# Performance work log

Hardware: AMD Instinct MI355X
Metric: run time of the kernel (lower is better)

Reference implementation:

```python
import jax, jax.numpy as jnp
import numpy as np

HEADS = 4
DH = 32            # hidden_state // multi_head = 128 // 4
HIDDEN = HEADS * DH
TEMP = float(HIDDEN) ** 0.5   # hidden_state ** alpha, alpha=0.5
BN_EPS = 1e-5


def _conv1x1(x, w, b):
    # x: [B,C,W,H], w: [O,C], b: [O] -> [B,O,W,H]
    y = jnp.einsum('oc,bcwh->bowh', w, x)
    return y + b[None, :, None, None]


def setup_inputs() -> dict:
    key = jax.random.key(0)
    ks = jax.random.split(key, 12)
    B, C, W, H = 2, 512, 64, 64
    s = lambda k, shape, scale=0.05: jax.random.normal(k, shape, jnp.float32) * scale
    return {
        'x': jax.random.normal(ks[0], (B, C, W, H), jnp.float32),
        'wq': s(ks[1], (HIDDEN, C)), 'bq': s(ks[2], (HIDDEN,)),
        'wk': s(ks[3], (HIDDEN, C)), 'bk': s(ks[4], (HIDDEN,)),
        'wv': s(ks[5], (HIDDEN, C)), 'bv': s(ks[6], (HIDDEN,)),
        'w_fuse': s(ks[7], (HEADS, HEADS), 0.5),
        'w_out': s(ks[8], (C, HIDDEN)), 'b_out': s(ks[9], (C,)),
        'bn_gamma': jnp.ones((C,), jnp.float32),
        'bn_beta': jnp.zeros((C,), jnp.float32),
        'bn_mean': s(ks[10], (C,), 0.1),
        'bn_var': jax.random.uniform(ks[11], (C,), jnp.float32, 0.5, 1.5),
    }


def reference(x, wq, bq, wk, bk, wv, bv, w_fuse, w_out, b_out,
              bn_gamma, bn_beta, bn_mean, bn_var):
    B, C, W, H = x.shape
    N = W * H
    # 1x1 conv QKV projections, split into heads
    q = _conv1x1(x, wq, bq).reshape(B, HEADS, DH, N)        # [B,h,d,N]
    q = jnp.swapaxes(q, 2, 3)                               # [B,h,N,d]
    k = _conv1x1(x, wk, bk).reshape(B, HEADS, DH, N)        # [B,h,d,N]
    v = jnp.swapaxes(_conv1x1(x, wv, bv).reshape(B, HEADS, DH, N), 2, 3)  # [B,h,N,d]
    # scaled dot-product scores
    attn = jnp.einsum('bhnd,bhdm->bhnm', q / jnp.float32(TEMP), k)  # [B,h,N,N]
    # fuse: 1x1 conv across heads on the score tensor (no bias)
    attn = jnp.einsum('gh,bhnm->bgnm', w_fuse, attn)
    attn = jax.nn.softmax(attn, axis=-1)
    # dropout is identity in eval mode
    out = jnp.einsum('bhnm,bhmd->bhnd', attn, v)            # [B,h,N,d]
    out = jnp.swapaxes(out, 2, 3).reshape(B, HIDDEN, W, H)
    out = _conv1x1(out, w_out, b_out)
    # BatchNorm2d in eval mode (running stats)
    inv = jax.lax.rsqrt(bn_var + BN_EPS)
    out = (out - bn_mean[None, :, None, None]) * (bn_gamma * inv)[None, :, None, None] \
          + bn_beta[None, :, None, None]
    return out, attn
```

## Files before the change

### kernel.cpp

```cpp
#include <hip/hip_runtime.h>
#include <hip/hip_bf16.h>
#include <cstdint>
#include <cstddef>

#define B_   2
#define C_   512
#define N_   4096
#define NH   4
#define DH_  32
#define HID  128
#define LOG2E 1.4426950408889634f

typedef __attribute__((ext_vector_type(8))) short bf16x8;
typedef __attribute__((ext_vector_type(4))) float f32x4;

#if __has_builtin(__builtin_amdgcn_exp2f)
#define EXP2(x) __builtin_amdgcn_exp2f(x)
#else
#define EXP2(x) exp2f(x)
#endif

static __device__ __forceinline__ unsigned short f2bf(float f) {
  union { float f; unsigned int u; } v; v.f = f;
  unsigned int r = v.u + 0x7fffu + ((v.u >> 16) & 1u);
  return (unsigned short)(r >> 16);
}

static __device__ __forceinline__ float sbc(float x) {
  return __uint_as_float(__builtin_amdgcn_readfirstlane(__float_as_uint(x)));
}

__global__ __launch_bounds__(256)
void prep_w(const float* __restrict__ wq, const float* __restrict__ wk,
            const float* __restrict__ wv, const float* __restrict__ wout,
            const float* __restrict__ bout, const float* __restrict__ gamma,
            const float* __restrict__ beta, const float* __restrict__ mean,
            const float* __restrict__ var,
            unsigned short* __restrict__ wbf,
            float* __restrict__ gsws, float* __restrict__ shws)
{
  if (blockIdx.x == 256) {
    int co = threadIdx.x;
#pragma unroll
    for (int i = 0; i < 2; i++, co += 256) {
      float gs = gamma[co] * rsqrtf(var[co] + 1e-5f);
      gsws[co] = gs;
      shws[co] = (bout[co] - mean[co]) * gs + beta[co];
    }
    return;
  }
  int gid  = blockIdx.x * 256 + threadIdx.x;
  int elem = gid * 4;
  int t    = elem >> 16;
  int off  = elem & 65535;
  const float* src = (t == 0) ? wq : (t == 1) ? wk : (t == 2) ? wv : wout;
  float4 v = *(const float4*)(src + off);
  alignas(8) unsigned short tmp[4];
  tmp[0] = f2bf(v.x); tmp[1] = f2bf(v.y); tmp[2] = f2bf(v.z); tmp[3] = f2bf(v.w);
  *(uint2*)(wbf + t * 65536 + off) = *(const uint2*)tmp;
}

__global__ __launch_bounds__(256)
void prep_xt(const float* __restrict__ x, unsigned short* __restrict__ xT)
{
  int bid = blockIdx.x;
  int b   = bid >> 9;
  int rem = bid & 511;
  int ct  = rem >> 6;
  int nt  = rem & 63;
  int c0  = ct << 6;
  int n0  = nt << 6;

  int tid = threadIdx.x;
  __shared__ float xs[64][65];

  const float* xb = x + (size_t)b * C_ * N_;
#pragma unroll
  for (int rr = 0; rr < 16; rr++) {
    int row = (tid >> 6) * 16 + rr;
    xs[row][tid & 63] = xb[(size_t)(c0 + row) * N_ + n0 + (tid & 63)];
  }
  __syncthreads();

  int cseg = (tid & 7) * 8;
#pragma unroll
  for (int pass = 0; pass < 2; pass++) {
    int nrow = pass * 32 + (tid >> 3);
    alignas(16) unsigned short tmp[8];
#pragma unroll
    for (int j = 0; j < 8; j++) tmp[j] = f2bf(xs[cseg + j][nrow]);
    *(uint4*)(xT + ((size_t)b * N_ + n0 + nrow) * C_ + c0 + cseg) = *(const uint4*)tmp;
  }
}

__global__ __launch_bounds__(256)
void qkv_gemm(const unsigned short* __restrict__ wbf,
              const unsigned short* __restrict__ xT,
              const float* __restrict__ bq, const float* __restrict__ bk,
              const float* __restrict__ bv,
              unsigned short* __restrict__ qws,
              unsigned short* __restrict__ kws,
              unsigned short* __restrict__ vtws)
{
  int bid = blockIdx.x;
  int ot  = bid % 6;
  int ntl = bid / 6;
  int b   = ntl >> 6;
  int n0  = (ntl & 63) << 6;
  int o0  = ot << 6;
  int t   = o0 >> 7;

  int tid = threadIdx.x;
  int w   = tid >> 6;
  int l   = tid & 63;
  int lg  = l >> 4;
  int lc  = l & 15;

  const unsigned short* xrow = xT + ((size_t)b * N_ + n0 + w * 16 + lc) * C_;
  const unsigned short* wrow0 = wbf + (size_t)(o0 + lc) * C_;

  const f32x4 zc = {0.f, 0.f, 0.f, 0.f};
  f32x4 acc[4] = {zc, zc, zc, zc};

  for (int k0 = 0; k0 < C_; k0 += 32) {
    bf16x8 bfrag = *(const bf16x8*)(xrow + k0 + lg * 8);
#pragma unroll
    for (int sub = 0; sub < 4; sub++) {
      bf16x8 afrag = *(const bf16x8*)(wrow0 + (size_t)sub * 16 * C_ + k0 + lg * 8);
      acc[sub] = __builtin_amdgcn_mfma_f32_16x16x32_bf16(afrag, bfrag, acc[sub], 0, 0, 0);
    }
  }

  const float* bias_t = (t == 0) ? bq : (t == 1) ? bk : bv;
  int n = n0 + w * 16 + lc;

#pragma unroll
  for (int sub = 0; sub < 4; sub++) {
    int oobase = (o0 & 127) + sub * 16;
    float4 bs = *(const float4*)(bias_t + oobase + lg * 4);
    float val[4];
    val[0] = acc[sub][0] + bs.x;
    val[1] = acc[sub][1] + bs.y;
    val[2] = acc[sub][2] + bs.z;
    val[3] = acc[sub][3] + bs.w;
    int h  = oobase >> 5;
    int d0 = (oobase & 31) + lg * 4;
    if (t < 2) {
      unsigned short* dst = (t == 0 ? qws : kws)
                          + (((size_t)(b * NH + h)) * N_ + n) * DH_ + d0;
      alignas(8) unsigned short tmp[4];
#pragma unroll
      for (int r = 0; r < 4; r++) tmp[r] = f2bf(val[r]);
      *(uint2*)dst = *(const uint2*)tmp;
    } else {
      unsigned short* dst = vtws + (((size_t)(b * NH + h)) * DH_ + d0) * N_ + n;
#pragma unroll
      for (int r = 0; r < 4; r++) dst[(size_t)r * N_] = f2bf(val[r]);
    }
  }
}

__global__ __launch_bounds__(512)
void attn_zpv(const unsigned short* __restrict__ qws,
              const unsigned short* __restrict__ kws,
              const unsigned short* __restrict__ vtws,
              const float* __restrict__ wfuse,
              const unsigned short* __restrict__ woutbf,
              const float* __restrict__ gsws, const float* __restrict__ shws,
              float* __restrict__ attn_out,
              float* __restrict__ out)
{
  int bid = blockIdx.x;
  int xcd = bid & 7;
  int b   = xcd >> 2;
  int qt  = (bid >> 3) * 4 + (xcd & 3);
  int n0  = qt << 4;

  int tid = threadIdx.x;
  int wv_ = tid >> 6;
  int l   = tid & 63;
  int lg  = l >> 4;
  int lc  = l & 15;

  __shared__ __align__(16) unsigned char lds_raw[8 * 4 * 16 * 40 * 2];
  unsigned short (*pbuf)[4][16][40] = (unsigned short (*)[4][16][40])lds_raw;
  float (*ored)[16][36] = (float (*)[16][36])lds_raw;
  unsigned short (*o128)[132] =
      (unsigned short (*)[132])(lds_raw + 20480);
  __shared__ float zred[8][4][4][4];

  const float TEMP = 11.313708498984761f;
  float wm[4][4];
#pragma unroll
  for (int g = 0; g < 4; g++)
#pragma unroll
    for (int h = 0; h < 4; h++)
      wm[g][h] = sbc(wfuse[g * 4 + h] * (LOG2E / TEMP));

  bf16x8 qf[4];
#pragma unroll
  for (int h = 0; h < 4; h++)
    qf[h] = *(const bf16x8*)(qws + (((size_t)(b * NH + h)) * N_ + n0 + lc) * DH_ + lg * 8);

  const f32x4 zc = {0.f, 0.f, 0.f, 0.f};

  float zp[4][4] = {};
#pragma unroll 1
  for (int pp = wv_; pp < 128; pp += 8) {
#pragma unroll
    for (int mm = 0; mm < 2; mm++) {
      int m0 = pp * 32 + mm * 16;
      f32x4 sh[4];
#pragma unroll
      for (int h = 0; h < 4; h++) {
        bf16x8 kf = *(const bf16x8*)(kws
            + (((size_t)(b * NH + h)) * N_ + m0 + lc) * DH_ + lg * 8);
        sh[h] = __builtin_amdgcn_mfma_f32_16x16x32_bf16(qf[h], kf, zc, 0, 0, 0);
      }
#pragma unroll
      for (int g = 0; g < 4; g++) {
        f32x4 sg = wm[g][0] * sh[0] + wm[g][1] * sh[1]
                 + wm[g][2] * sh[2] + wm[g][3] * sh[3];
#pragma unroll
        for (int r = 0; r < 4; r++) zp[g][r] += EXP2(sg[r]);
      }
    }
  }

#pragma unroll
  for (int g = 0; g < 4; g++)
#pragma unroll
    for (int r = 0; r < 4; r++) {
      float v = zp[g][r];
      v += __shfl_xor(v, 1, 16);
      v += __shfl_xor(v, 2, 16);
      v += __shfl_xor(v, 4, 16);
      v += __shfl_xor(v, 8, 16);
      zp[g][r] = v;
    }
  if (lc == 0) {
#pragma unroll
    for (int g = 0; g < 4; g++)
#pragma unroll
      for (int r = 0; r < 4; r++) zred[wv_][g][lg][r] = zp[g][r];
  }
  __syncthreads();

  float invZ[4][4];
#pragma unroll
  for (int g = 0; g < 4; g++)
#pragma unroll
    for (int r = 0; r < 4; r++) {
      float z = 0.f;
#pragma unroll
      for (int w = 0; w < 8; w++) z += zred[w][g][lg][r];
      invZ[g][r] = 1.0f / z;
    }

  f32x4 opv[4][2];
#pragma unroll
  for (int g = 0; g < 4; g++) { opv[g][0] = zc; opv[g][1] = zc; }

  float* attn_b = attn_out + (size_t)b * NH * N_ * N_;

  bf16x8 kf[2][4];
  {
    int m0p = wv_ * 32;
#pragma unroll
    for (int mm = 0; mm < 2; mm++)
#pragma unroll
      for (int h = 0; h < 4; h++)
        kf[mm][h] = *(const bf16x8*)(kws
            + (((size_t)(b * NH + h)) * N_ + m0p + mm * 16 + lc) * DH_ + lg * 8);
  }

#pragma unroll 1
  for (int pp = wv_; pp < 128; pp += 8) {
    int m0p = pp * 32;
    int ppn = pp + 8;
    int m0n = (ppn < 128 ? ppn : pp) * 32;

    bf16x8 kn[2][4];
#pragma unroll
    for (int mm = 0; mm < 2; mm++)
#pragma unroll
      for (int h = 0; h < 4; h++)
        kn[mm][h] = *(const bf16x8*)(kws
            + (((size_t)(b * NH + h)) * N_ + m0n + mm * 16 + lc) * DH_ + lg * 8);

#pragma unroll
    for (int mm = 0; mm < 2; mm++) {
      f32x4 sh[4];
#pragma unroll
      for (int h = 0; h < 4; h++)
        sh[h] = __builtin_amdgcn_mfma_f32_16x16x32_bf16(qf[h], kf[mm][h], zc, 0, 0, 0);
#pragma unroll
      for (int g = 0; g < 4; g++) {
        f32x4 sg = wm[g][0] * sh[0] + wm[g][1] * sh[1]
                 + wm[g][2] * sh[2] + wm[g][3] * sh[3];
#pragma unroll
        for (int r = 0; r < 4; r++) {
          float p = EXP2(sg[r]) * invZ[g][r];
          pbuf[wv_][g][lg * 4 + r][mm * 16 + lc] = f2bf(p);
        }
      }
    }

#pragma unroll
    for (int g = 0; g < 4; g++) {
      bf16x8 pa = *(const bf16x8*)(&pbuf[wv_][g][lc][lg * 8]);
#pragma unroll
      for (int dh = 0; dh < 2; dh++) {
        bf16x8 vb = *(const bf16x8*)(vtws
            + (((size_t)(b * NH + g)) * DH_ + dh * 16 + lc) * N_ + m0p + lg * 8);
        opv[g][dh] = __builtin_amdgcn_mfma_f32_16x16x32_bf16(pa, vb, opv[g][dh], 0, 0, 0);
      }
    }

#pragma unroll
    for (int it = 0; it < 8; it++) {
      int flat = it * 64 + l;
      int g   = flat >> 7;
      int row = (flat >> 3) & 15;
      int seg = flat & 7;
      uint2 pk = *(const uint2*)(&pbuf[wv_][g][row][seg * 4]);
      f32x4 o4;
      o4[0] = __uint_as_float(pk.x << 16);
      o4[1] = __uint_as_float(pk.x & 0xffff0000u);
      o4[2] = __uint_as_float(pk.y << 16);
      o4[3] = __uint_as_float(pk.y & 0xffff0000u);
      __builtin_nontemporal_store(o4,
          (f32x4*)(attn_b + ((size_t)g * N_ + n0 + row) * N_ + m0p + seg * 4));
    }

#pragma unroll
    for (int mm = 0; mm < 2; mm++)
#pragma unroll
      for (int h = 0; h < 4; h++)
        kf[mm][h] = kn[mm][h];
  }

  __syncthreads();

  int row2 = tid & 15;
  int d2   = tid >> 4;
#pragma unroll
  for (int g = 0; g < 4; g++) {
#pragma unroll
    for (int dh = 0; dh < 2; dh++)
#pragma unroll
      for (int r = 0; r < 4; r++)
        ored[wv_][lg * 4 + r][dh * 16 + lc] = opv[g][dh][r];
    __syncthreads();
    float s = 0.f;
#pragma unroll
    for (int w = 0; w < 8; w++) s += ored[w][row2][d2];
    o128[row2][g * 32 + d2] = f2bf(s);
    __syncthreads();
  }

  int cb = wv_ * 64;
  f32x4 oacc[4] = {zc, zc, zc, zc};
#pragma unroll
  for (int kk = 0; kk < 4; kk++) {
    bf16x8 bfrag = *(const bf16x8*)(&o128[lc][kk * 32 + lg * 8]);
#pragma unroll
    for (int sub = 0; sub < 4; sub++) {
      bf16x8 afrag = *(const bf16x8*)(woutbf
          + (size_t)(cb + sub * 16 + lc) * HID + kk * 32 + lg * 8);
      oacc[sub] = __builtin_amdgcn_mfma_f32_16x16x32_bf16(afrag, bfrag, oacc[sub], 0, 0, 0);
    }
  }

  float* outb = out + (size_t)b * C_ * N_;
#pragma unroll
  for (int sub = 0; sub < 4; sub++) {
    int co0 = cb + sub * 16 + lg * 4;
    float4 g4 = *(const float4*)(gsws + co0);
    float4 s4 = *(const float4*)(shws + co0);
    outb[(size_t)(co0 + 0) * N_ + n0 + lc] = oacc[sub][0] * g4.x + s4.x;
    outb[(size_t)(co0 + 1) * N_ + n0 + lc] = oacc[sub][1] * g4.y + s4.y;
    outb[(size_t)(co0 + 2) * N_ + n0 + lc] = oacc[sub][2] * g4.z + s4.z;
    outb[(size_t)(co0 + 3) * N_ + n0 + lc] = oacc[sub][3] * g4.w + s4.w;
  }
}

extern "C" void kernel_launch(void* const* d_in, const int* in_sizes, int n_in,
                              void* d_out, int out_size, void* d_ws, size_t ws_size,
                              hipStream_t stream)
{
  const float* x     = (const float*)d_in[0];
  const float* wq    = (const float*)d_in[1];
  const float* bq    = (const float*)d_in[2];
  const float* wk    = (const float*)d_in[3];
  const float* bk    = (const float*)d_in[4];
  const float* wv    = (const float*)d_in[5];
  const float* bv    = (const float*)d_in[6];
  const float* wfuse = (const float*)d_in[7];
  const float* wout  = (const float*)d_in[8];
  const float* bout  = (const float*)d_in[9];
  const float* gamma = (const float*)d_in[10];
  const float* beta  = (const float*)d_in[11];
  const float* mean  = (const float*)d_in[12];
  const float* var   = (const float*)d_in[13];

  const size_t QK_ELEMS = (size_t)B_ * NH * N_ * DH_;
  char* base = (char*)d_ws;
  unsigned short* qws  = (unsigned short*)base;
  unsigned short* kws  = qws + QK_ELEMS;
  unsigned short* vtws = kws + QK_ELEMS;
  unsigned short* xT   = (unsigned short*)(base + 3 * QK_ELEMS * sizeof(unsigned short));
  unsigned short* wbf  = (unsigned short*)(base + 3 * QK_ELEMS * sizeof(unsigned short)
                                           + (size_t)B_ * N_ * C_ * sizeof(unsigned short));
  unsigned short* woutbf = wbf + 3 * 65536;
  float* gsws = (float*)(wbf + 4 * 65536);
  float* shws = gsws + C_;

  float* out_f  = (float*)d_out;
  float* attn_f = out_f + (size_t)B_ * C_ * N_;

  hipLaunchKernelGGL(prep_w,   dim3(257),  dim3(256), 0, stream,
                     wq, wk, wv, wout, bout, gamma, beta, mean, var,
                     wbf, gsws, shws);
  hipLaunchKernelGGL(prep_xt,  dim3(1024), dim3(256), 0, stream, x, xT);
  hipLaunchKernelGGL(qkv_gemm, dim3(768),  dim3(256), 0, stream,
                     wbf, xT, bq, bk, bv, qws, kws, vtws);
  hipLaunchKernelGGL(attn_zpv, dim3(512), dim3(512), 0, stream,
                     qws, kws, vtws, wfuse, woutbf, gsws, shws, attn_f, out_f);
}
```

Before: 228.1 us.

## Fuse x transpose and bf16 conversion into QKV GEMM via LDS staging

Removes the separate prep_xt kernel and its bf16 transposed workspace; qkv_gemm now loads fp32 x tiles directly, stages them through double-buffered shared memory with register prefetch, and converts to bf16 when building the MFMA B fragment. This eliminates one launch and the write/read of the transposed activation buffer. In exchange each output-tile block re-reads fp32 x (twice the bytes of bf16, repeated across six o-tiles) and does redundant conversion work per block.

```diff
diff --git a/kernel.cpp b/kernel.cpp
--- a/kernel.cpp
+++ b/kernel.cpp
@@ -61,41 +61,8 @@
 }
 
 __global__ __launch_bounds__(256)
-void prep_xt(const float* __restrict__ x, unsigned short* __restrict__ xT)
-{
-  int bid = blockIdx.x;
-  int b   = bid >> 9;
-  int rem = bid & 511;
-  int ct  = rem >> 6;
-  int nt  = rem & 63;
-  int c0  = ct << 6;
-  int n0  = nt << 6;
-
-  int tid = threadIdx.x;
-  __shared__ float xs[64][65];
-
-  const float* xb = x + (size_t)b * C_ * N_;
-#pragma unroll
-  for (int rr = 0; rr < 16; rr++) {
-    int row = (tid >> 6) * 16 + rr;
-    xs[row][tid & 63] = xb[(size_t)(c0 + row) * N_ + n0 + (tid & 63)];
-  }
-  __syncthreads();
-
-  int cseg = (tid & 7) * 8;
-#pragma unroll
-  for (int pass = 0; pass < 2; pass++) {
-    int nrow = pass * 32 + (tid >> 3);
-    alignas(16) unsigned short tmp[8];
-#pragma unroll
-    for (int j = 0; j < 8; j++) tmp[j] = f2bf(xs[cseg + j][nrow]);
-    *(uint4*)(xT + ((size_t)b * N_ + n0 + nrow) * C_ + c0 + cseg) = *(const uint4*)tmp;
-  }
-}
-
-__global__ __launch_bounds__(256)
 void qkv_gemm(const unsigned short* __restrict__ wbf,
-              const unsigned short* __restrict__ xT,
+              const float* __restrict__ x,
               const float* __restrict__ bq, const float* __restrict__ bk,
               const float* __restrict__ bv,
               unsigned short* __restrict__ qws,
@@ -116,14 +83,41 @@
   int lg  = l >> 4;
   int lc  = l & 15;
 
-  const unsigned short* xrow = xT + ((size_t)b * N_ + n0 + w * 16 + lc) * C_;
+  __shared__ float xs[2][32][65];
+
+  int nn    = tid & 63;
+  int rbase = tid >> 6;
+
+  const float* xb = x + (size_t)b * C_ * N_ + n0;
   const unsigned short* wrow0 = wbf + (size_t)(o0 + lc) * C_;
+
+  float xr[8];
+#pragma unroll
+  for (int p = 0; p < 8; p++)
+    xr[p] = xb[(size_t)(p * 4 + rbase) * N_ + nn];
 
   const f32x4 zc = {0.f, 0.f, 0.f, 0.f};
   f32x4 acc[4] = {zc, zc, zc, zc};
 
-  for (int k0 = 0; k0 < C_; k0 += 32) {
-    bf16x8 bfrag = *(const bf16x8*)(xrow + k0 + lg * 8);
+#pragma unroll 1
+  for (int step = 0; step < 16; step++) {
+    int buf = step & 1;
+#pragma unroll
+    for (int p = 0; p < 8; p++)
+      xs[buf][p * 4 + rbase][nn] = xr[p];
+    __syncthreads();
+    if (step < 15) {
+      int k0n = (step + 1) * 32;
+#pragma unroll
+      for (int p = 0; p < 8; p++)
+        xr[p] = xb[(size_t)(k0n + p * 4 + rbase) * N_ + nn];
+    }
+    int k0 = step * 32;
+    alignas(16) unsigned short bt[8];
+#pragma unroll
+    for (int j = 0; j < 8; j++)
+      bt[j] = f2bf(xs[buf][lg * 8 + j][w * 16 + lc]);
+    bf16x8 bfrag = *(const bf16x8*)bt;
 #pragma unroll
     for (int sub = 0; sub < 4; sub++) {
       bf16x8 afrag = *(const bf16x8*)(wrow0 + (size_t)sub * 16 * C_ + k0 + lg * 8);
@@ -409,9 +403,7 @@
   unsigned short* qws  = (unsigned short*)base;
   unsigned short* kws  = qws + QK_ELEMS;
   unsigned short* vtws = kws + QK_ELEMS;
-  unsigned short* xT   = (unsigned short*)(base + 3 * QK_ELEMS * sizeof(unsigned short));
-  unsigned short* wbf  = (unsigned short*)(base + 3 * QK_ELEMS * sizeof(unsigned short)
-                                           + (size_t)B_ * N_ * C_ * sizeof(unsigned short));
+  unsigned short* wbf  = (unsigned short*)(base + 3 * QK_ELEMS * sizeof(unsigned short));
   unsigned short* woutbf = wbf + 3 * 65536;
   float* gsws = (float*)(wbf + 4 * 65536);
   float* shws = gsws + C_;
@@ -422,9 +414,8 @@
   hipLaunchKernelGGL(prep_w,   dim3(257),  dim3(256), 0, stream,
                      wq, wk, wv, wout, bout, gamma, beta, mean, var,
                      wbf, gsws, shws);
-  hipLaunchKernelGGL(prep_xt,  dim3(1024), dim3(256), 0, stream, x, xT);
   hipLaunchKernelGGL(qkv_gemm, dim3(768),  dim3(256), 0, stream,
-                     wbf, xT, bq, bk, bv, qws, kws, vtws);
+                     wbf, x, bq, bk, bv, qws, kws, vtws);
   hipLaunchKernelGGL(attn_zpv, dim3(512), dim3(512), 0, stream,
                      qws, kws, vtws, wfuse, woutbf, gsws, shws, attn_f, out_f);
 }
```

Result: faster. 223.0 us (-2.3%).
